# Performance work log

Measured on AMD Instinct MI355X. Metric: run time of the kernel, lower is better.

The kernel has to match this reference:

```python
import jax, jax.numpy as jnp
import numpy as np

B_SZ, H_DIM, W_DIM, D_MODEL = 2, 64, 64, 192
N_STATE = 16   # d_state
R_RANK = 12    # dt_rank
K_DIRS = 4
LN_EPS = 1e-5


def setup_inputs() -> dict:
    key = jax.random.key(0)
    ks = jax.random.split(key, 5)
    x = jax.random.normal(ks[0], (B_SZ, H_DIM, W_DIM, D_MODEL), jnp.float32)
    # x_proj Linear weights, small init so dt/B/C projections stay numerically tame
    x_proj_weight = jax.random.normal(ks[1], (K_DIRS, R_RANK + 2 * N_STATE, D_MODEL), jnp.float32) * 0.02
    # dt_proj weight ~ U(-rank^-0.5, rank^-0.5) as in dt_init('random')
    dt_projs_weight = jax.random.uniform(ks[2], (K_DIRS, D_MODEL, R_RANK), jnp.float32,
                                         -(R_RANK ** -0.5), R_RANK ** -0.5)
    # dt bias = inverse-softplus of dt sampled log-uniform in [1e-3, 0.1]
    dt = jnp.exp(jax.random.uniform(ks[3], (K_DIRS, D_MODEL)) * (np.log(0.1) - np.log(1e-3)) + np.log(1e-3))
    dt = jnp.clip(dt, 1e-4, None)
    dt_projs_bias = dt + jnp.log(-jnp.expm1(-dt))
    # A_log_init: log(arange(1..N)) tiled over K*D rows
    A_logs = jnp.log(jnp.tile(jnp.arange(1, N_STATE + 1, dtype=jnp.float32), (K_DIRS * D_MODEL, 1)))
    Ds = jnp.ones((K_DIRS * D_MODEL,), jnp.float32)
    ln_weight = jnp.ones((D_MODEL,), jnp.float32)
    ln_bias = jnp.zeros((D_MODEL,), jnp.float32)
    return dict(x=x, x_proj_weight=x_proj_weight, dt_projs_weight=dt_projs_weight,
                dt_projs_bias=dt_projs_bias, A_logs=A_logs, Ds=Ds,
                ln_weight=ln_weight, ln_bias=ln_bias)


def _cross_scan(x):  # x: (B, D, H, W) -> (B, 4, D, L)
    b, d, h, w = x.shape
    x0 = x.reshape(b, d, h * w)                                  # row-major scan
    x1 = jnp.transpose(x, (0, 1, 3, 2)).reshape(b, d, h * w)     # column-major scan
    xs = jnp.stack([x0, x1], axis=1)
    return jnp.concatenate([xs, jnp.flip(xs, axis=-1)], axis=1)  # + both reversed


def _cross_merge(ys, h, w):  # ys: (B, 4, D, L) -> (B, D, L)
    b, _, d, l = ys.shape
    ys = ys[:, 0:2] + jnp.flip(ys[:, 2:4], axis=-1)
    y1 = jnp.transpose(ys[:, 1].reshape(b, d, w, h), (0, 1, 3, 2)).reshape(b, d, l)
    return ys[:, 0] + y1


def _selective_scan(xs, dts, A, Bs, Cs):
    # xs, dts: (B, K, D, L); A: (K, D, N); Bs, Cs: (B, K, N, L). dts already softplus'd.
    b, k, d, l = xs.shape
    n = A.shape[-1]

    @jax.checkpoint
    def step(h_prev, t):
        x_t, dt_t, B_t, C_t = t                         # (B,K,D),(B,K,D),(B,K,N),(B,K,N)
        dA = jnp.exp(dt_t[..., None] * A)               # (B,K,D,N)
        dBx = (dt_t * x_t)[..., None] * B_t[:, :, None, :]
        h = dA * h_prev + dBx
        y = jnp.einsum('bkdn,bkn->bkd', h, C_t)
        return h, y

    seq = (jnp.moveaxis(xs, -1, 0), jnp.moveaxis(dts, -1, 0),
           jnp.moveaxis(Bs, -1, 0), jnp.moveaxis(Cs, -1, 0))
    h0 = jnp.zeros((b, k, d, n), xs.dtype)
    _, ys = jax.lax.scan(step, h0, seq)                 # ys: (L,B,K,D)
    return jnp.moveaxis(ys, 0, -1)                      # (B,K,D,L)


def reference(x, x_proj_weight, dt_projs_weight, dt_projs_bias, A_logs, Ds, ln_weight, ln_bias):
    b, h, w, d = x.shape
    l = h * w
    xc = jnp.transpose(x, (0, 3, 1, 2))                  # (B, D, H, W)
    xs = _cross_scan(xc)                                 # (B, K, D, L)
    x_dbl = jnp.einsum('bkdl,kcd->bkcl', xs, x_proj_weight)
    dts, Bs, Cs = jnp.split(x_dbl, [R_RANK, R_RANK + N_STATE], axis=2)
    dts = jnp.einsum('bkrl,kdr->bkdl', dts, dt_projs_weight)
    dts = jax.nn.softplus(dts + dt_projs_bias[None, :, :, None])   # delta_softplus + bias
    A = -jnp.exp(A_logs).reshape(K_DIRS, d, N_STATE)
    ys = _selective_scan(xs, dts, A, Bs, Cs)             # (B, K, D, L)
    ys = ys + Ds.reshape(1, K_DIRS, d, 1) * xs           # D skip connection
    y = _cross_merge(ys, h, w)                           # (B, D, L)
    y = jnp.transpose(y, (0, 2, 1))                      # (B, L, D)
    mu = jnp.mean(y, -1, keepdims=True)
    var = jnp.mean(jnp.square(y - mu), -1, keepdims=True)
    y = (y - mu) * jax.lax.rsqrt(var + LN_EPS) * ln_weight + ln_bias   # out_norm LayerNorm
    return y.reshape(b, h, w, d)
```

## Files before the change

### kernel.cpp

```cpp
#include <hip/hip_runtime.h>
#include <math.h>

#define B_SZ 2
#define HH 64
#define WW 64
#define DM 192
#define NS 16
#define RR 12
#define KD 4
#define LL (HH * WW)
#define CPROJ (RR + 2 * NS)
#define CPAD 48
#define SCH 16
#define TLP 64
#define LOG2E 1.44269504088896340736f
#define LN2F 0.69314718055994530942f

__device__ __forceinline__ int spatial_idx(int k, int t) {
    if (k == 0) return t;
    if (k == 1) return ((t & 63) << 6) | (t >> 6);
    if (k == 2) return LL - 1 - t;
    int tp = LL - 1 - t;
    return ((tp & 63) << 6) | (tp >> 6);
}

__global__ __launch_bounds__(256) void proj_kernel(const float* __restrict__ x,
                                                   const float* __restrict__ xpw,
                                                   float* __restrict__ xdbl) {
    int blk = blockIdx.x;
    int ltile = blk % (LL / TLP);
    int bk = blk / (LL / TLP);
    int k = bk & 3;
    int b = bk >> 2;
    int l0 = ltile * TLP;

    __shared__ float xt[DM * (TLP + 1)];

    {
        int li = threadIdx.x >> 2;
        int d0 = (threadIdx.x & 3) * 48;
        int s = spatial_idx(k, l0 + li);
        const float4* xr = (const float4*)(x + ((size_t)b * LL + s) * DM + d0);
#pragma unroll
        for (int q = 0; q < 12; ++q) {
            float4 v = xr[q];
            int d = d0 + q * 4;
            xt[(d + 0) * (TLP + 1) + li] = v.x;
            xt[(d + 1) * (TLP + 1) + li] = v.y;
            xt[(d + 2) * (TLP + 1) + li] = v.z;
            xt[(d + 3) * (TLP + 1) + li] = v.w;
        }
    }
    __syncthreads();

    int lane = threadIdx.x & 63;
    int wv = threadIdx.x >> 6;
    int c0 = __builtin_amdgcn_readfirstlane(wv * 11);
    const float* wk = xpw + (size_t)k * CPROJ * DM;

    float acc[11];
#pragma unroll
    for (int ci = 0; ci < 11; ++ci) acc[ci] = 0.f;

    for (int d = 0; d < DM; ++d) {
        float xv = xt[d * (TLP + 1) + lane];
#pragma unroll
        for (int ci = 0; ci < 11; ++ci)
            acc[ci] = fmaf(xv, wk[(size_t)(c0 + ci) * DM + d], acc[ci]);
    }
    float* orow = xdbl + ((size_t)bk * LL + l0 + lane) * CPAD;
#pragma unroll
    for (int ci = 0; ci < 11; ++ci) orow[c0 + ci] = acc[ci];
}

template <int PHASE, int NCHT, int ATOMIC>
__global__ __launch_bounds__(192) void scan_kernel(
    const float* __restrict__ x, const float* __restrict__ xdbl,
    const float* __restrict__ dtw, const float* __restrict__ dtb,
    const float* __restrict__ Alogs, const float* __restrict__ Ds,
    float* __restrict__ carry, float* __restrict__ aprod, float* __restrict__ ybuf) {
    const int CHT = LL / NCHT;
    int blk = blockIdx.x;
    int chunk = blk % NCHT;
    int bk = blk / NCHT;
    int k = bk & 3;
    int b = bk >> 2;
    int d = threadIdx.x;
    int kd = k * DM + d;

    float Wdt[RR];
#pragma unroll
    for (int r = 0; r < RR; ++r) Wdt[r] = dtw[(size_t)kd * RR + r];
    float bias = dtb[kd];
    float Avl2[NS];
#pragma unroll
    for (int n = 0; n < NS; ++n) Avl2[n] = -__expf(Alogs[(size_t)kd * NS + n]) * LOG2E;
    float Dval = Ds[kd];

    bool pws = true;
#pragma unroll
    for (int n = 0; n < NS; ++n)
        pws = pws && (fabsf(Avl2[n] - (float)(n + 1) * Avl2[0]) <= 1e-5f * fabsf(Avl2[n]) + 1e-30f);
    const bool pw = (__all(pws ? 1 : 0) != 0);

    float h[NS];
    float dtsum = 0.f;
    size_t cbase = ((size_t)(bk * NCHT + chunk) * DM + d) * NS;
    if (PHASE == 1) {
#pragma unroll
        for (int n = 0; n < NS; ++n) h[n] = 0.f;
    } else {
#pragma unroll
        for (int n = 0; n < NS; ++n) h[n] = carry[cbase + n];
    }

    __shared__ float lds[SCH * CPAD];
    int tbase = chunk * CHT;
    for (int t0 = tbase; t0 < tbase + CHT; t0 += SCH) {
        __syncthreads();
        for (int i = threadIdx.x; i < SCH * CPAD; i += DM)
            lds[i] = xdbl[((size_t)bk * LL + t0) * CPAD + i];
        __syncthreads();
        for (int tt = 0; tt < SCH; ++tt) {
            const float* row = lds + tt * CPAD;
            int t = t0 + tt;
            float z = bias;
#pragma unroll
            for (int r = 0; r < RR; ++r) z = fmaf(row[r], Wdt[r], z);
            float dt = (z > 15.f) ? z : __log2f(1.f + exp2f(z * LOG2E)) * LN2F;
            int s = spatial_idx(k, t);
            float xv = x[((size_t)b * LL + s) * DM + d];
            float dtx = dt * xv;

            float dA[NS];
            if (pw) {
                float e1 = exp2f(dt * Avl2[0]);
                dA[0] = e1;
                dA[1] = e1 * e1;
                dA[2] = dA[1] * e1;
                dA[3] = dA[1] * dA[1];
                dA[4] = dA[3] * e1;
                dA[5] = dA[3] * dA[1];
                dA[6] = dA[3] * dA[2];
                dA[7] = dA[3] * dA[3];
                dA[8] = dA[7] * e1;
                dA[9] = dA[7] * dA[1];
                dA[10] = dA[7] * dA[2];
                dA[11] = dA[7] * dA[3];
                dA[12] = dA[7] * dA[4];
                dA[13] = dA[7] * dA[5];
                dA[14] = dA[7] * dA[6];
                dA[15] = dA[7] * dA[7];
            } else {
#pragma unroll
                for (int n = 0; n < NS; ++n) dA[n] = exp2f(dt * Avl2[n]);
            }

            float y = 0.f;
#pragma unroll
            for (int n = 0; n < NS; ++n) {
                h[n] = fmaf(dA[n], h[n], dtx * row[RR + n]);
                if (PHASE == 3) y = fmaf(h[n], row[RR + NS + n], y);
            }
            if (PHASE == 1) dtsum += dt;
            if (PHASE == 3) {
                float val = y + Dval * xv;
                size_t oidx = ((size_t)b * LL + s) * DM + d;
                if (ATOMIC) atomicAdd(&ybuf[oidx], val);
                else        ybuf[(size_t)k * (B_SZ * LL * DM) + oidx] = val;
            }
        }
    }
    if (PHASE == 1) {
#pragma unroll
        for (int n = 0; n < NS; ++n) {
            carry[cbase + n] = h[n];
            aprod[cbase + n] = exp2f(dtsum * Avl2[n]);
        }
    }
}

template <int NCHT>
__global__ __launch_bounds__(256) void fix_kernel(float* __restrict__ carry,
                                                  const float* __restrict__ aprod) {
    int idx = blockIdx.x * 256 + threadIdx.x;
    int n = idx & (NS - 1);
    int dn = idx >> 4;
    int d = dn % DM;
    int bk = dn / DM;
    size_t base = ((size_t)bk * NCHT * DM + d) * NS + n;
    const size_t stride = (size_t)DM * NS;
    float hp = 0.f;
    for (int c = 0; c < NCHT; ++c) {
        size_t off = base + (size_t)c * stride;
        float P = aprod[off];
        float Cr = carry[off];
        carry[off] = hp;
        hp = fmaf(P, hp, Cr);
    }
}

template <int NB>
__global__ __launch_bounds__(256) void ln_kernel(const float* __restrict__ ybuf,
                                                 const float* __restrict__ lnw,
                                                 const float* __restrict__ lnb,
                                                 float* __restrict__ out) {
    const size_t SEG = (size_t)B_SZ * LL * DM;
    int row = blockIdx.x * 4 + (threadIdx.x >> 6);
    int lane = threadIdx.x & 63;
    const float* yr = ybuf + (size_t)row * DM;
    float v0 = 0.f, v1 = 0.f, v2 = 0.f;
#pragma unroll
    for (int kq = 0; kq < NB; ++kq) {
        const float* p = yr + kq * SEG;
        v0 += p[lane];
        v1 += p[lane + 64];
        v2 += p[lane + 128];
    }
    float s = v0 + v1 + v2;
    float sq = v0 * v0 + v1 * v1 + v2 * v2;
#pragma unroll
    for (int off = 32; off >= 1; off >>= 1) {
        s += __shfl_xor(s, off, 64);
        sq += __shfl_xor(sq, off, 64);
    }
    float mu = s * (1.f / DM);
    float var = sq * (1.f / DM) - mu * mu;
    float inv = rsqrtf(var + 1e-5f);
    float* orow = out + (size_t)row * DM;
    orow[lane]       = (v0 - mu) * inv * lnw[lane]       + lnb[lane];
    orow[lane + 64]  = (v1 - mu) * inv * lnw[lane + 64]  + lnb[lane + 64];
    orow[lane + 128] = (v2 - mu) * inv * lnw[lane + 128] + lnb[lane + 128];
}

__global__ __launch_bounds__(256) void zero_kernel(float4* __restrict__ p, int n4) {
    for (int i = blockIdx.x * 256 + threadIdx.x; i < n4; i += gridDim.x * 256)
        p[i] = make_float4(0.f, 0.f, 0.f, 0.f);
}

extern "C" void kernel_launch(void* const* d_in, const int* in_sizes, int n_in,
                              void* d_out, int out_size, void* d_ws, size_t ws_size,
                              hipStream_t stream) {
    const float* x    = (const float*)d_in[0];
    const float* xpw  = (const float*)d_in[1];
    const float* dtw  = (const float*)d_in[2];
    const float* dtb  = (const float*)d_in[3];
    const float* Alog = (const float*)d_in[4];
    const float* Ds   = (const float*)d_in[5];
    const float* lnw  = (const float*)d_in[6];
    const float* lnb  = (const float*)d_in[7];
    float* out = (float*)d_out;

    const size_t F_XD   = (size_t)B_SZ * KD * LL * CPAD;
    const size_t F_C64  = (size_t)B_SZ * KD * 64 * DM * NS;
    const size_t F_C128 = 2 * F_C64;
    const size_t F_YB   = (size_t)B_SZ * LL * DM;

    float* ws   = (float*)d_ws;
    float* xdbl = ws;

    proj_kernel<<<B_SZ * KD * (LL / TLP), 256, 0, stream>>>(x, xpw, xdbl);

    if (ws_size >= (F_XD + 2 * F_C128 + 4 * F_YB) * sizeof(float)) {
        float* carry = xdbl + F_XD;
        float* aprod = carry + F_C128;
        float* ybuf4 = aprod + F_C128;
        scan_kernel<1, 128, 0><<<B_SZ * KD * 128, DM, 0, stream>>>(x, xdbl, dtw, dtb, Alog, Ds,
                                                                   carry, aprod, ybuf4);
        fix_kernel<128><<<(B_SZ * KD * DM * NS) / 256, 256, 0, stream>>>(carry, aprod);
        scan_kernel<3, 128, 0><<<B_SZ * KD * 128, DM, 0, stream>>>(x, xdbl, dtw, dtb, Alog, Ds,
                                                                   carry, aprod, ybuf4);
        ln_kernel<4><<<(B_SZ * LL) / 4, 256, 0, stream>>>(ybuf4, lnw, lnb, out);
    } else {
        float* carry = xdbl + F_XD;
        float* aprod = carry + F_C128;
        float* ybuf  = aprod;
        scan_kernel<1, 128, 1><<<B_SZ * KD * 128, DM, 0, stream>>>(x, xdbl, dtw, dtb, Alog, Ds,
                                                                   carry, aprod, ybuf);
        fix_kernel<128><<<(B_SZ * KD * DM * NS) / 256, 256, 0, stream>>>(carry, aprod);
        zero_kernel<<<1024, 256, 0, stream>>>((float4*)ybuf, (int)(F_YB / 4));
        scan_kernel<3, 128, 1><<<B_SZ * KD * 128, DM, 0, stream>>>(x, xdbl, dtw, dtb, Alog, Ds,
                                                                   carry, aprod, ybuf);
        ln_kernel<1><<<(B_SZ * LL) / 4, 256, 0, stream>>>(ybuf, lnw, lnb, out);
    }
}
```

Measured before the change: 94.45 us.

## Fuse chunked scan phases into one cooperative kernel with grid syncs

Replaces the separate phase-1 scan, carry-fix and phase-3 scan launches with a single cooperative kernel that uses grid.sync between phases. The chunk count drops from 128 to 64 so all 512 blocks can be co-resident, and each block stages its whole chunk of projections into LDS once and reuses it in phase 3. Rows are read as float4 vectors. This removes launch gaps and the repeated xdbl reloads, at the cost of half the parallelism per scan, longer serial chunks and grid-wide barrier overhead. A fallback three-kernel path is kept in case the cooperative launch fails.

```diff
diff --git a/kernel.cpp b/kernel.cpp
--- a/kernel.cpp
+++ b/kernel.cpp
@@ -1,5 +1,8 @@
 #include <hip/hip_runtime.h>
+#include <hip/hip_cooperative_groups.h>
 #include <math.h>
+
+namespace cg = cooperative_groups;
 
 #define B_SZ 2
 #define HH 64
@@ -11,10 +14,15 @@
 #define LL (HH * WW)
 #define CPROJ (RR + 2 * NS)
 #define CPAD 48
-#define SCH 16
+#define NCHc 64
+#define CHc (LL / NCHc)
+#define NBLK (B_SZ * KD * NCHc)
 #define TLP 64
 #define LOG2E 1.44269504088896340736f
 #define LN2F 0.69314718055994530942f
+
+#define RQF(arr, i) (((i) & 3) == 0 ? arr[(i) >> 2].x : ((i) & 3) == 1 ? arr[(i) >> 2].y \
+                     : ((i) & 3) == 2 ? arr[(i) >> 2].z : arr[(i) >> 2].w)
 
 __device__ __forceinline__ int spatial_idx(int k, int t) {
     if (k == 0) return t;
@@ -22,6 +30,217 @@
     if (k == 2) return LL - 1 - t;
     int tp = LL - 1 - t;
     return ((tp & 63) << 6) | (tp >> 6);
+}
+
+__device__ __forceinline__ void compute_dA(float dt, const float* Avl2, bool pw, float* dA) {
+    if (pw) {
+        float e1 = exp2f(dt * Avl2[0]);
+        dA[0] = e1;
+        dA[1] = e1 * e1;
+        dA[2] = dA[1] * e1;
+        dA[3] = dA[1] * dA[1];
+        dA[4] = dA[3] * e1;
+        dA[5] = dA[3] * dA[1];
+        dA[6] = dA[3] * dA[2];
+        dA[7] = dA[3] * dA[3];
+        dA[8] = dA[7] * e1;
+        dA[9] = dA[7] * dA[1];
+        dA[10] = dA[7] * dA[2];
+        dA[11] = dA[7] * dA[3];
+        dA[12] = dA[7] * dA[4];
+        dA[13] = dA[7] * dA[5];
+        dA[14] = dA[7] * dA[6];
+        dA[15] = dA[7] * dA[7];
+    } else {
+#pragma unroll
+        for (int n = 0; n < NS; ++n) dA[n] = exp2f(dt * Avl2[n]);
+    }
+}
+
+__device__ __forceinline__ void load_params(int kd, const float* __restrict__ dtw,
+                                            const float* __restrict__ dtb,
+                                            const float* __restrict__ Alogs,
+                                            float* Wdt, float& bias, float* Avl2, bool& pw) {
+#pragma unroll
+    for (int r = 0; r < RR; ++r) Wdt[r] = dtw[(size_t)kd * RR + r];
+    bias = dtb[kd];
+#pragma unroll
+    for (int n = 0; n < NS; ++n) Avl2[n] = -__expf(Alogs[(size_t)kd * NS + n]) * LOG2E;
+    bool pws = true;
+#pragma unroll
+    for (int n = 0; n < NS; ++n)
+        pws = pws && (fabsf(Avl2[n] - (float)(n + 1) * Avl2[0]) <= 1e-5f * fabsf(Avl2[n]) + 1e-30f);
+    pw = (__all(pws ? 1 : 0) != 0);
+}
+
+__device__ __forceinline__ void scan_phase1_dev(
+    int blk, int tid, const float* __restrict__ x, const float* __restrict__ xdbl,
+    const float* __restrict__ dtw, const float* __restrict__ dtb,
+    const float* __restrict__ Alogs,
+    float* __restrict__ carry, float* __restrict__ aprod, float* xds) {
+    const int chunk = blk % NCHc;
+    const int bk = blk / NCHc;
+    const int k = bk & 3, b = bk >> 2;
+    const int d = tid;
+    float Wdt[RR], bias, Avl2[NS];
+    bool pw;
+    load_params(k * DM + d, dtw, dtb, Alogs, Wdt, bias, Avl2, pw);
+
+    {
+        float4* dst = (float4*)xds;
+        const float4* src = (const float4*)(xdbl + ((size_t)bk * LL + chunk * CHc) * CPAD);
+#pragma unroll
+        for (int i = 0; i < CHc * CPAD / 4 / DM; ++i)
+            dst[tid + i * DM] = src[tid + i * DM];
+    }
+    __syncthreads();
+
+    const float* xb = x + (size_t)b * LL * DM + d;
+    float h[NS];
+#pragma unroll
+    for (int n = 0; n < NS; ++n) h[n] = 0.f;
+    float dtsum = 0.f;
+
+#pragma unroll 4
+    for (int tt = 0; tt < CHc; ++tt) {
+        const float4* row4 = (const float4*)(xds + tt * CPAD);
+        float4 rq[7];
+#pragma unroll
+        for (int q = 0; q < 7; ++q) rq[q] = row4[q];
+        float z = bias;
+#pragma unroll
+        for (int r = 0; r < RR; ++r) z = fmaf(RQF(rq, r), Wdt[r], z);
+        float dt = (z > 15.f) ? z : __log2f(1.f + exp2f(z * LOG2E)) * LN2F;
+        int s = spatial_idx(k, chunk * CHc + tt);
+        float xv = xb[(size_t)s * DM];
+        float dtx = dt * xv;
+        dtsum += dt;
+        float dA[NS];
+        compute_dA(dt, Avl2, pw, dA);
+#pragma unroll
+        for (int n = 0; n < NS; ++n)
+            h[n] = fmaf(dA[n], h[n], dtx * RQF(rq, RR + n));
+    }
+    const size_t cbase = ((size_t)blk * DM + d) * NS;
+#pragma unroll
+    for (int n = 0; n < NS; ++n) {
+        carry[cbase + n] = h[n];
+        aprod[cbase + n] = exp2f(dtsum * Avl2[n]);
+    }
+}
+
+__device__ __forceinline__ void fix_dev(int idx, float* __restrict__ carry,
+                                        const float* __restrict__ aprod) {
+    int n = idx & (NS - 1);
+    int dn = idx >> 4;
+    int dd = dn % DM;
+    int bkc = dn / DM;
+    size_t base = ((size_t)bkc * NCHc * DM + dd) * NS + n;
+    const size_t stride = (size_t)DM * NS;
+    float hp = 0.f;
+#pragma unroll 4
+    for (int c = 0; c < NCHc; ++c) {
+        size_t off = base + (size_t)c * stride;
+        float P = aprod[off];
+        float Cr = carry[off];
+        carry[off] = hp;
+        hp = fmaf(P, hp, Cr);
+    }
+}
+
+template <bool STAGE>
+__device__ __forceinline__ void scan_phase3_dev(
+    int blk, int tid, const float* __restrict__ x, const float* __restrict__ xdbl,
+    const float* __restrict__ dtw, const float* __restrict__ dtb,
+    const float* __restrict__ Alogs, const float* __restrict__ Ds,
+    const float* __restrict__ carry, float* __restrict__ ybuf4, float* xds) {
+    const int chunk = blk % NCHc;
+    const int bk = blk / NCHc;
+    const int k = bk & 3, b = bk >> 2;
+    const int d = tid;
+    float Wdt[RR], bias, Avl2[NS];
+    bool pw;
+    load_params(k * DM + d, dtw, dtb, Alogs, Wdt, bias, Avl2, pw);
+    const float Dval = Ds[k * DM + d];
+
+    if (STAGE) {
+        float4* dst = (float4*)xds;
+        const float4* src = (const float4*)(xdbl + ((size_t)bk * LL + chunk * CHc) * CPAD);
+#pragma unroll
+        for (int i = 0; i < CHc * CPAD / 4 / DM; ++i)
+            dst[tid + i * DM] = src[tid + i * DM];
+        __syncthreads();
+    }
+
+    const float* xb = x + (size_t)b * LL * DM + d;
+    const size_t cbase = ((size_t)blk * DM + d) * NS;
+    float h[NS];
+#pragma unroll
+    for (int n = 0; n < NS; ++n) h[n] = carry[cbase + n];
+    float* yk = ybuf4 + (size_t)k * ((size_t)B_SZ * LL * DM) + (size_t)b * LL * DM + d;
+
+#pragma unroll 4
+    for (int tt = 0; tt < CHc; ++tt) {
+        const float4* row4 = (const float4*)(xds + tt * CPAD);
+        float4 rq[11];
+#pragma unroll
+        for (int q = 0; q < 11; ++q) rq[q] = row4[q];
+        float z = bias;
+#pragma unroll
+        for (int r = 0; r < RR; ++r) z = fmaf(RQF(rq, r), Wdt[r], z);
+        float dt = (z > 15.f) ? z : __log2f(1.f + exp2f(z * LOG2E)) * LN2F;
+        int s = spatial_idx(k, chunk * CHc + tt);
+        float xv = xb[(size_t)s * DM];
+        float dtx = dt * xv;
+        float dA[NS];
+        compute_dA(dt, Avl2, pw, dA);
+        float y = 0.f;
+#pragma unroll
+        for (int n = 0; n < NS; ++n) {
+            h[n] = fmaf(dA[n], h[n], dtx * RQF(rq, RR + n));
+            y = fmaf(h[n], RQF(rq, RR + NS + n), y);
+        }
+        yk[(size_t)s * DM] = y + Dval * xv;
+    }
+}
+
+__global__ __launch_bounds__(192) void scan_coop(
+    const float* __restrict__ x, const float* __restrict__ xdbl,
+    const float* __restrict__ dtw, const float* __restrict__ dtb,
+    const float* __restrict__ Alogs, const float* __restrict__ Ds,
+    float* __restrict__ carry, float* __restrict__ aprod, float* __restrict__ ybuf4) {
+    __shared__ float xds[CHc * CPAD];
+    cg::grid_group grid = cg::this_grid();
+    scan_phase1_dev(blockIdx.x, threadIdx.x, x, xdbl, dtw, dtb, Alogs, carry, aprod, xds);
+    grid.sync();
+    if (blockIdx.x < 128)
+        fix_dev(blockIdx.x * DM + threadIdx.x, carry, aprod);
+    grid.sync();
+    scan_phase3_dev<false>(blockIdx.x, threadIdx.x, x, xdbl, dtw, dtb, Alogs, Ds,
+                           carry, ybuf4, xds);
+}
+
+__global__ __launch_bounds__(192) void scan1_kernel(
+    const float* __restrict__ x, const float* __restrict__ xdbl,
+    const float* __restrict__ dtw, const float* __restrict__ dtb,
+    const float* __restrict__ Alogs, float* __restrict__ carry, float* __restrict__ aprod) {
+    __shared__ float xds[CHc * CPAD];
+    scan_phase1_dev(blockIdx.x, threadIdx.x, x, xdbl, dtw, dtb, Alogs, carry, aprod, xds);
+}
+
+__global__ __launch_bounds__(192) void fix_kernel(float* __restrict__ carry,
+                                                  const float* __restrict__ aprod) {
+    fix_dev(blockIdx.x * DM + threadIdx.x, carry, aprod);
+}
+
+__global__ __launch_bounds__(192) void scan3_kernel(
+    const float* __restrict__ x, const float* __restrict__ xdbl,
+    const float* __restrict__ dtw, const float* __restrict__ dtb,
+    const float* __restrict__ Alogs, const float* __restrict__ Ds,
+    const float* __restrict__ carry, float* __restrict__ ybuf4) {
+    __shared__ float xds[CHc * CPAD];
+    scan_phase3_dev<true>(blockIdx.x, threadIdx.x, x, xdbl, dtw, dtb, Alogs, Ds,
+                          carry, ybuf4, xds);
 }
 
 __global__ __launch_bounds__(256) void proj_kernel(const float* __restrict__ x,
@@ -73,134 +292,6 @@
     for (int ci = 0; ci < 11; ++ci) orow[c0 + ci] = acc[ci];
 }
 
-template <int PHASE, int NCHT, int ATOMIC>
-__global__ __launch_bounds__(192) void scan_kernel(
-    const float* __restrict__ x, const float* __restrict__ xdbl,
-    const float* __restrict__ dtw, const float* __restrict__ dtb,
-    const float* __restrict__ Alogs, const float* __restrict__ Ds,
-    float* __restrict__ carry, float* __restrict__ aprod, float* __restrict__ ybuf) {
-    const int CHT = LL / NCHT;
-    int blk = blockIdx.x;
-    int chunk = blk % NCHT;
-    int bk = blk / NCHT;
-    int k = bk & 3;
-    int b = bk >> 2;
-    int d = threadIdx.x;
-    int kd = k * DM + d;
-
-    float Wdt[RR];
-#pragma unroll
-    for (int r = 0; r < RR; ++r) Wdt[r] = dtw[(size_t)kd * RR + r];
-    float bias = dtb[kd];
-    float Avl2[NS];
-#pragma unroll
-    for (int n = 0; n < NS; ++n) Avl2[n] = -__expf(Alogs[(size_t)kd * NS + n]) * LOG2E;
-    float Dval = Ds[kd];
-
-    bool pws = true;
-#pragma unroll
-    for (int n = 0; n < NS; ++n)
-        pws = pws && (fabsf(Avl2[n] - (float)(n + 1) * Avl2[0]) <= 1e-5f * fabsf(Avl2[n]) + 1e-30f);
-    const bool pw = (__all(pws ? 1 : 0) != 0);
-
-    float h[NS];
-    float dtsum = 0.f;
-    size_t cbase = ((size_t)(bk * NCHT + chunk) * DM + d) * NS;
-    if (PHASE == 1) {
-#pragma unroll
-        for (int n = 0; n < NS; ++n) h[n] = 0.f;
-    } else {
-#pragma unroll
-        for (int n = 0; n < NS; ++n) h[n] = carry[cbase + n];
-    }
-
-    __shared__ float lds[SCH * CPAD];
-    int tbase = chunk * CHT;
-    for (int t0 = tbase; t0 < tbase + CHT; t0 += SCH) {
-        __syncthreads();
-        for (int i = threadIdx.x; i < SCH * CPAD; i += DM)
-            lds[i] = xdbl[((size_t)bk * LL + t0) * CPAD + i];
-        __syncthreads();
-        for (int tt = 0; tt < SCH; ++tt) {
-            const float* row = lds + tt * CPAD;
-            int t = t0 + tt;
-            float z = bias;
-#pragma unroll
-            for (int r = 0; r < RR; ++r) z = fmaf(row[r], Wdt[r], z);
-            float dt = (z > 15.f) ? z : __log2f(1.f + exp2f(z * LOG2E)) * LN2F;
-            int s = spatial_idx(k, t);
-            float xv = x[((size_t)b * LL + s) * DM + d];
-            float dtx = dt * xv;
-
-            float dA[NS];
-            if (pw) {
-                float e1 = exp2f(dt * Avl2[0]);
-                dA[0] = e1;
-                dA[1] = e1 * e1;
-                dA[2] = dA[1] * e1;
-                dA[3] = dA[1] * dA[1];
-                dA[4] = dA[3] * e1;
-                dA[5] = dA[3] * dA[1];
-                dA[6] = dA[3] * dA[2];
-                dA[7] = dA[3] * dA[3];
-                dA[8] = dA[7] * e1;
-                dA[9] = dA[7] * dA[1];
-                dA[10] = dA[7] * dA[2];
-                dA[11] = dA[7] * dA[3];
-                dA[12] = dA[7] * dA[4];
-                dA[13] = dA[7] * dA[5];
-                dA[14] = dA[7] * dA[6];
-                dA[15] = dA[7] * dA[7];
-            } else {
-#pragma unroll
-                for (int n = 0; n < NS; ++n) dA[n] = exp2f(dt * Avl2[n]);
-            }
-
-            float y = 0.f;
-#pragma unroll
-            for (int n = 0; n < NS; ++n) {
-                h[n] = fmaf(dA[n], h[n], dtx * row[RR + n]);
-                if (PHASE == 3) y = fmaf(h[n], row[RR + NS + n], y);
-            }
-            if (PHASE == 1) dtsum += dt;
-            if (PHASE == 3) {
-                float val = y + Dval * xv;
-                size_t oidx = ((size_t)b * LL + s) * DM + d;
-                if (ATOMIC) atomicAdd(&ybuf[oidx], val);
-                else        ybuf[(size_t)k * (B_SZ * LL * DM) + oidx] = val;
-            }
-        }
-    }
-    if (PHASE == 1) {
-#pragma unroll
-        for (int n = 0; n < NS; ++n) {
-            carry[cbase + n] = h[n];
-            aprod[cbase + n] = exp2f(dtsum * Avl2[n]);
-        }
-    }
-}
-
-template <int NCHT>
-__global__ __launch_bounds__(256) void fix_kernel(float* __restrict__ carry,
-                                                  const float* __restrict__ aprod) {
-    int idx = blockIdx.x * 256 + threadIdx.x;
-    int n = idx & (NS - 1);
-    int dn = idx >> 4;
-    int d = dn % DM;
-    int bk = dn / DM;
-    size_t base = ((size_t)bk * NCHT * DM + d) * NS + n;
-    const size_t stride = (size_t)DM * NS;
-    float hp = 0.f;
-    for (int c = 0; c < NCHT; ++c) {
-        size_t off = base + (size_t)c * stride;
-        float P = aprod[off];
-        float Cr = carry[off];
-        carry[off] = hp;
-        hp = fmaf(P, hp, Cr);
-    }
-}
-
-template <int NB>
 __global__ __launch_bounds__(256) void ln_kernel(const float* __restrict__ ybuf,
                                                  const float* __restrict__ lnw,
                                                  const float* __restrict__ lnb,
@@ -211,7 +302,7 @@
     const float* yr = ybuf + (size_t)row * DM;
     float v0 = 0.f, v1 = 0.f, v2 = 0.f;
 #pragma unroll
-    for (int kq = 0; kq < NB; ++kq) {
+    for (int kq = 0; kq < KD; ++kq) {
         const float* p = yr + kq * SEG;
         v0 += p[lane];
         v1 += p[lane + 64];
@@ -231,11 +322,6 @@
     orow[lane]       = (v0 - mu) * inv * lnw[lane]       + lnb[lane];
     orow[lane + 64]  = (v1 - mu) * inv * lnw[lane + 64]  + lnb[lane + 64];
     orow[lane + 128] = (v2 - mu) * inv * lnw[lane + 128] + lnb[lane + 128];
-}
-
-__global__ __launch_bounds__(256) void zero_kernel(float4* __restrict__ p, int n4) {
-    for (int i = blockIdx.x * 256 + threadIdx.x; i < n4; i += gridDim.x * 256)
-        p[i] = make_float4(0.f, 0.f, 0.f, 0.f);
 }
 
 extern "C" void kernel_launch(void* const* d_in, const int* in_sizes, int n_in,
@@ -251,36 +337,29 @@
     const float* lnb  = (const float*)d_in[7];
     float* out = (float*)d_out;
 
-    const size_t F_XD   = (size_t)B_SZ * KD * LL * CPAD;
-    const size_t F_C64  = (size_t)B_SZ * KD * 64 * DM * NS;
-    const size_t F_C128 = 2 * F_C64;
-    const size_t F_YB   = (size_t)B_SZ * LL * DM;
-
-    float* ws   = (float*)d_ws;
-    float* xdbl = ws;
+    const size_t F_XD = (size_t)B_SZ * KD * LL * CPAD;
+    const size_t F_CR = (size_t)B_SZ * KD * NCHc * DM * NS;
+    const size_t F_YB = (size_t)B_SZ * LL * DM;
+
+    float* ws    = (float*)d_ws;
+    float* xdbl  = ws;
+    float* carry = xdbl + F_XD;
+    float* aprod = carry + F_CR;
+    float* ybuf4 = aprod + F_CR;
 
     proj_kernel<<<B_SZ * KD * (LL / TLP), 256, 0, stream>>>(x, xpw, xdbl);
 
-    if (ws_size >= (F_XD + 2 * F_C128 + 4 * F_YB) * sizeof(float)) {
-        float* carry = xdbl + F_XD;
-        float* aprod = carry + F_C128;
-        float* ybuf4 = aprod + F_C128;
-        scan_kernel<1, 128, 0><<<B_SZ * KD * 128, DM, 0, stream>>>(x, xdbl, dtw, dtb, Alog, Ds,
-                                                                   carry, aprod, ybuf4);
-        fix_kernel<128><<<(B_SZ * KD * DM * NS) / 256, 256, 0, stream>>>(carry, aprod);
-        scan_kernel<3, 128, 0><<<B_SZ * KD * 128, DM, 0, stream>>>(x, xdbl, dtw, dtb, Alog, Ds,
-                                                                   carry, aprod, ybuf4);
-        ln_kernel<4><<<(B_SZ * LL) / 4, 256, 0, stream>>>(ybuf4, lnw, lnb, out);
-    } else {
-        float* carry = xdbl + F_XD;
-        float* aprod = carry + F_C128;
-        float* ybuf  = aprod;
-        scan_kernel<1, 128, 1><<<B_SZ * KD * 128, DM, 0, stream>>>(x, xdbl, dtw, dtb, Alog, Ds,
-                                                                   carry, aprod, ybuf);
-        fix_kernel<128><<<(B_SZ * KD * DM * NS) / 256, 256, 0, stream>>>(carry, aprod);
-        zero_kernel<<<1024, 256, 0, stream>>>((float4*)ybuf, (int)(F_YB / 4));
-        scan_kernel<3, 128, 1><<<B_SZ * KD * 128, DM, 0, stream>>>(x, xdbl, dtw, dtb, Alog, Ds,
-                                                                   carry, aprod, ybuf);
-        ln_kernel<1><<<(B_SZ * LL) / 4, 256, 0, stream>>>(ybuf, lnw, lnb, out);
-    }
-}
+    void* args[] = { (void*)&x, (void*)&xdbl, (void*)&dtw, (void*)&dtb,
+                     (void*)&Alog, (void*)&Ds, (void*)&carry, (void*)&aprod,
+                     (void*)&ybuf4 };
+    hipError_t cerr = hipLaunchCooperativeKernel((const void*)scan_coop, dim3(NBLK), dim3(DM),
+                                                 args, 0, stream);
+    if (cerr != hipSuccess) {
+        (void)hipGetLastError();
+        scan1_kernel<<<NBLK, DM, 0, stream>>>(x, xdbl, dtw, dtb, Alog, carry, aprod);
+        fix_kernel<<<128, DM, 0, stream>>>(carry, aprod);
+        scan3_kernel<<<NBLK, DM, 0, stream>>>(x, xdbl, dtw, dtb, Alog, Ds, carry, ybuf4);
+    }
+
+    ln_kernel<<<(B_SZ * LL) / 4, 256, 0, stream>>>(ybuf4, lnw, lnb, out);
+}
```

Measured after the change: 243.9 us. 2.58x slower.
